# Kernel optimization log

Hardware: AMD Instinct MI355X
Metric: run time of the kernel (lower is better)

## Reference

```python
import jax, jax.numpy as jnp
import numpy as np

BATCH = 65536
IN_A = 256
IN_B = 256
OUT = 64


def setup_inputs() -> dict:
    key = jax.random.key(0)
    k1, k2, k3, k4 = jax.random.split(key, 4)
    xa = jax.random.normal(k1, (BATCH, IN_A), dtype=jnp.float32)
    xb = jax.random.normal(k2, (BATCH, IN_B), dtype=jnp.float32)
    wa = jax.random.normal(k3, (IN_A, OUT), dtype=jnp.float32) * 0.05
    wb = jax.random.normal(k4, (IN_B, OUT), dtype=jnp.float32) * 0.05
    return {"xa": xa, "xb": xb, "wa": wa, "wb": wb}


def reference(xa, xb, wa, wb):
    # Plaintext semantics of the SSHE cross secret-shared matmul:
    # [z|rank_b] = [xa|rank_a] @ <wa> + [xb|rank_b] @ <wb>
    return xa @ wa + xb @ wb
```

## Files before the change

kernel.cpp:

```cpp
#include <hip/hip_runtime.h>
#include <stdint.h>


#define BATCH     65536
#define KH        256
#define NOUT      64
#define WT_SHORTS (512 * 64)
#define WT_BYTES  (WT_SHORTS * 2)

typedef __bf16 bf16x8 __attribute__((ext_vector_type(8)));
typedef float  f32x4  __attribute__((ext_vector_type(4)));


__global__ void prep_wt_kernel(const float* __restrict__ wa,
                               const float* __restrict__ wb,
                               __bf16* __restrict__ wt) {
    int t = blockIdx.x * 256 + threadIdx.x;
    int c = t & 63;
    int k = t >> 6;
    float va = wa[k * 64 + c];
    float vb = wb[k * 64 + c];
    int k2 = k + 256;
    wt[(k  >> 3) * 512 + c * 8 + (k  & 7)] = (__bf16)va;
    wt[(k2 >> 3) * 512 + c * 8 + (k2 & 7)] = (__bf16)vb;
}

template <bool USE_WS>
__global__ __launch_bounds__(512, 4)
void agg_gemm_kernel(const float* __restrict__ xa,
                     const float* __restrict__ xb,
                     const float* __restrict__ wa,
                     const float* __restrict__ wb,
                     const __bf16* __restrict__ wt,
                     float* __restrict__ out) {
    __shared__ __bf16 wlds[WT_SHORTS];
    const int t    = threadIdx.x;
    const int lane = t & 63;
    const int wave = t >> 6;

    if (USE_WS) {
        const f32x4* gsrc = (const f32x4*)wt;
        f32x4*       ldst = (f32x4*)&wlds[0];
        #pragma unroll
        for (int it = 0; it < 8; ++it) {
            ldst[it * 512 + t] = gsrc[it * 512 + t];
        }
    } else {
        int c  = t & 63;
        int kw = t >> 6;
        #pragma unroll
        for (int i = 0; i < 32; ++i) {
            int k  = kw * 32 + i;
            int k2 = k + 256;
            wlds[(k  >> 3) * 512 + c * 8 + (k  & 7)] = (__bf16)wa[k * 64 + c];
            wlds[(k2 >> 3) * 512 + c * 8 + (k2 & 7)] = (__bf16)wb[k * 64 + c];
        }
    }
    __syncthreads();

    const int gw   = blockIdx.x * 8 + wave;
    const int row  = gw * 16 + (lane & 15);
    const int kgrp = lane >> 4;
    const int kk   = kgrp * 8;

    const float* pa = xa + (size_t)row * 256 + kk;
    const float* pb = xb + (size_t)row * 256 + kk;

    f32x4 acc0 = {0.f, 0.f, 0.f, 0.f};
    f32x4 acc1 = acc0, acc2 = acc0, acc3 = acc0;

    #pragma unroll
    for (int step = 0; step < 16; ++step) {
        const int k0 = step * 32;
        const float* px = (step < 8) ? (pa + k0) : (pb + (k0 - 256));
        f32x4 x0 = *(const f32x4*)(px);
        f32x4 x1 = *(const f32x4*)(px + 4);
        bf16x8 af;
        af[0] = (__bf16)x0[0]; af[1] = (__bf16)x0[1];
        af[2] = (__bf16)x0[2]; af[3] = (__bf16)x0[3];
        af[4] = (__bf16)x1[0]; af[5] = (__bf16)x1[1];
        af[6] = (__bf16)x1[2]; af[7] = (__bf16)x1[3];

        const __bf16* bbase = &wlds[(step * 4 + kgrp) * 512 + (lane & 15) * 8];
        bf16x8 b0 = *(const bf16x8*)(bbase);
        bf16x8 b1 = *(const bf16x8*)(bbase + 16 * 8);
        bf16x8 b2 = *(const bf16x8*)(bbase + 32 * 8);
        bf16x8 b3 = *(const bf16x8*)(bbase + 48 * 8);

        acc0 = __builtin_amdgcn_mfma_f32_16x16x32_bf16(af, b0, acc0, 0, 0, 0);
        acc1 = __builtin_amdgcn_mfma_f32_16x16x32_bf16(af, b1, acc1, 0, 0, 0);
        acc2 = __builtin_amdgcn_mfma_f32_16x16x32_bf16(af, b2, acc2, 0, 0, 0);
        acc3 = __builtin_amdgcn_mfma_f32_16x16x32_bf16(af, b3, acc3, 0, 0, 0);
    }

    const int oc = lane & 15;
    float* po = out + (size_t)(gw * 16 + (lane >> 4) * 4) * 64 + oc;
    #pragma unroll
    for (int r = 0; r < 4; ++r) {
        po[r * 64 +  0] = acc0[r];
        po[r * 64 + 16] = acc1[r];
        po[r * 64 + 32] = acc2[r];
        po[r * 64 + 48] = acc3[r];
    }
}

extern "C" void kernel_launch(void* const* d_in, const int* in_sizes, int n_in,
                              void* d_out, int out_size, void* d_ws, size_t ws_size,
                              hipStream_t stream) {
    const float* xa = (const float*)d_in[0];
    const float* xb = (const float*)d_in[1];
    const float* wa = (const float*)d_in[2];
    const float* wb = (const float*)d_in[3];
    float* out = (float*)d_out;

    if (ws_size >= (size_t)WT_BYTES) {
        __bf16* wt = (__bf16*)d_ws;
        prep_wt_kernel<<<64, 256, 0, stream>>>(wa, wb, wt);
        agg_gemm_kernel<true><<<512, 512, 0, stream>>>(xa, xb, wa, wb, wt, out);
    } else {
        agg_gemm_kernel<false><<<512, 512, 0, stream>>>(xa, xb, wa, wb, nullptr, out);
    }
}
```

Baseline: 163.2 us.

## Stream activation tiles into LDS via async global_load_lds with double buffering

Activation rows are no longer loaded straight into registers from global memory. Each wave now stages 16x64-float chunks into a per-wave XOR-swizzled LDS buffer using global_load_lds, double buffered, with explicit vmcnt waits so the next chunk's loads overlap the MFMAs on the current one. The aim is better coalescing and latency hiding for the bandwidth-bound activation stream. In exchange it adds 64KB of LDS per block and drops the 4-block occupancy hint, so fewer blocks may be resident per CU.

New measurement: 159.2 us. -2.5%, faster.

```diff
diff --git a/kernel.cpp b/kernel.cpp
--- a/kernel.cpp
+++ b/kernel.cpp
@@ -2,15 +2,11 @@
 #include <stdint.h>
 
 
-#define BATCH     65536
-#define KH        256
-#define NOUT      64
 #define WT_SHORTS (512 * 64)
 #define WT_BYTES  (WT_SHORTS * 2)
 
 typedef __bf16 bf16x8 __attribute__((ext_vector_type(8)));
 typedef float  f32x4  __attribute__((ext_vector_type(4)));
-
 
 __global__ void prep_wt_kernel(const float* __restrict__ wa,
                                const float* __restrict__ wb,
@@ -25,15 +21,23 @@
     wt[(k2 >> 3) * 512 + c * 8 + (k2 & 7)] = (__bf16)vb;
 }
 
+__device__ __forceinline__ void gload16(const void* g, void* l) {
+    __builtin_amdgcn_global_load_lds(
+        (const __attribute__((address_space(1))) void*)g,
+        (__attribute__((address_space(3))) void*)l, 16, 0, 0);
+}
+
 template <bool USE_WS>
-__global__ __launch_bounds__(512, 4)
+__global__ __launch_bounds__(512)
 void agg_gemm_kernel(const float* __restrict__ xa,
                      const float* __restrict__ xb,
                      const float* __restrict__ wa,
                      const float* __restrict__ wb,
                      const __bf16* __restrict__ wt,
                      float* __restrict__ out) {
-    __shared__ __bf16 wlds[WT_SHORTS];
+    __shared__ __align__(16) __bf16 wlds[WT_SHORTS];
+    __shared__ __align__(16) float xlds[2 * 8 * 1024];
+
     const int t    = threadIdx.x;
     const int lane = t & 63;
     const int wave = t >> 6;
@@ -42,9 +46,8 @@
         const f32x4* gsrc = (const f32x4*)wt;
         f32x4*       ldst = (f32x4*)&wlds[0];
         #pragma unroll
-        for (int it = 0; it < 8; ++it) {
+        for (int it = 0; it < 8; ++it)
             ldst[it * 512 + t] = gsrc[it * 512 + t];
-        }
     } else {
         int c  = t & 63;
         int kw = t >> 6;
@@ -59,42 +62,73 @@
     __syncthreads();
 
     const int gw   = blockIdx.x * 8 + wave;
-    const int row  = gw * 16 + (lane & 15);
+    const int tile = gw * 16;
+    const int row  = lane & 15;
     const int kgrp = lane >> 4;
-    const int kk   = kgrp * 8;
+    const int sw   = (row & 7) << 4;
 
-    const float* pa = xa + (size_t)row * 256 + kk;
-    const float* pb = xb + (size_t)row * 256 + kk;
+    char* xw0 = (char*)&xlds[(0 * 8 + wave) * 1024];
+    char* xw1 = (char*)&xlds[(1 * 8 + wave) * 1024];
+
+    const int r_lo = lane >> 4;
+    const int fk4  = (lane & 15) * 4;
+    auto stage = [&](int c) {
+        const float* srcm = (c < 4) ? xa : xb;
+        const int k0 = (c & 3) * 64;
+        char* ldsb = (c & 1) ? xw1 : xw0;
+        #pragma unroll
+        for (int j = 0; j < 4; ++j) {
+            int r = j * 4 + r_lo;
+            int f = fk4 ^ ((r & 7) << 2);
+            const float* g = srcm + (size_t)(tile + r) * 256 + k0 + f;
+            gload16(g, ldsb + j * 1024);
+        }
+    };
+
+    stage(0);
+    stage(1);
 
     f32x4 acc0 = {0.f, 0.f, 0.f, 0.f};
     f32x4 acc1 = acc0, acc2 = acc0, acc3 = acc0;
 
     #pragma unroll
-    for (int step = 0; step < 16; ++step) {
-        const int k0 = step * 32;
-        const float* px = (step < 8) ? (pa + k0) : (pb + (k0 - 256));
-        f32x4 x0 = *(const f32x4*)(px);
-        f32x4 x1 = *(const f32x4*)(px + 4);
-        bf16x8 af;
-        af[0] = (__bf16)x0[0]; af[1] = (__bf16)x0[1];
-        af[2] = (__bf16)x0[2]; af[3] = (__bf16)x0[3];
-        af[4] = (__bf16)x1[0]; af[5] = (__bf16)x1[1];
-        af[6] = (__bf16)x1[2]; af[7] = (__bf16)x1[3];
+    for (int c = 0; c < 8; ++c) {
+        if (c < 7) asm volatile("s_waitcnt vmcnt(4)" ::: "memory");
+        else       asm volatile("s_waitcnt vmcnt(0)" ::: "memory");
 
-        const __bf16* bbase = &wlds[(step * 4 + kgrp) * 512 + (lane & 15) * 8];
-        bf16x8 b0 = *(const bf16x8*)(bbase);
-        bf16x8 b1 = *(const bf16x8*)(bbase + 16 * 8);
-        bf16x8 b2 = *(const bf16x8*)(bbase + 32 * 8);
-        bf16x8 b3 = *(const bf16x8*)(bbase + 48 * 8);
+        const char* xbb = (c & 1) ? xw1 : xw0;
+        #pragma unroll
+        for (int sub = 0; sub < 2; ++sub) {
+            const int step = c * 2 + sub;
+            const int b0   = row * 256 + sub * 128 + kgrp * 32;
+            f32x4 x0 = *(const f32x4*)(xbb + (b0 ^ sw));
+            f32x4 x1 = *(const f32x4*)(xbb + ((b0 + 16) ^ sw));
+            bf16x8 af;
+            af[0] = (__bf16)x0[0]; af[1] = (__bf16)x0[1];
+            af[2] = (__bf16)x0[2]; af[3] = (__bf16)x0[3];
+            af[4] = (__bf16)x1[0]; af[5] = (__bf16)x1[1];
+            af[6] = (__bf16)x1[2]; af[7] = (__bf16)x1[3];
 
-        acc0 = __builtin_amdgcn_mfma_f32_16x16x32_bf16(af, b0, acc0, 0, 0, 0);
-        acc1 = __builtin_amdgcn_mfma_f32_16x16x32_bf16(af, b1, acc1, 0, 0, 0);
-        acc2 = __builtin_amdgcn_mfma_f32_16x16x32_bf16(af, b2, acc2, 0, 0, 0);
-        acc3 = __builtin_amdgcn_mfma_f32_16x16x32_bf16(af, b3, acc3, 0, 0, 0);
+            const __bf16* bbase = &wlds[(step * 4 + kgrp) * 512 + row * 8];
+            bf16x8 bf0 = *(const bf16x8*)(bbase);
+            bf16x8 bf1 = *(const bf16x8*)(bbase + 128);
+            bf16x8 bf2 = *(const bf16x8*)(bbase + 256);
+            bf16x8 bf3 = *(const bf16x8*)(bbase + 384);
+
+            acc0 = __builtin_amdgcn_mfma_f32_16x16x32_bf16(af, bf0, acc0, 0, 0, 0);
+            acc1 = __builtin_amdgcn_mfma_f32_16x16x32_bf16(af, bf1, acc1, 0, 0, 0);
+            acc2 = __builtin_amdgcn_mfma_f32_16x16x32_bf16(af, bf2, acc2, 0, 0, 0);
+            acc3 = __builtin_amdgcn_mfma_f32_16x16x32_bf16(af, bf3, acc3, 0, 0, 0);
+        }
+
+        if (c < 6) {
+            asm volatile("s_waitcnt lgkmcnt(0)" ::: "memory");
+            __builtin_amdgcn_sched_barrier(0);
+            stage(c + 2);
+        }
     }
 
-    const int oc = lane & 15;
-    float* po = out + (size_t)(gw * 16 + (lane >> 4) * 4) * 64 + oc;
+    float* po = out + (size_t)(tile + kgrp * 4) * 64 + row;
     #pragma unroll
     for (int r = 0; r < 4; ++r) {
         po[r * 64 +  0] = acc0[r];
```

## Prefetch activation rows four steps ahead and relayout weights for contiguous LDS reads

Applied to the files above, without the earlier changes.

The weight prep now writes the bf16 weights in exactly the per-lane fragment order the MFMA loop consumes, so each lane reads four contiguous 16-byte chunks at lane*8 offsets instead of a strided pattern. The main loop keeps a 4-deep register ring of activation loads, issuing global loads four k-steps ahead so memory latency overlaps the MFMAs. This costs extra VGPRs for the prefetch buffer, which may pressure occupancy under the 512x4 launch bounds.

Result: no change. 162.3 us (-0.6%).

```diff
diff --git a/kernel.cpp b/kernel.cpp
--- a/kernel.cpp
+++ b/kernel.cpp
@@ -2,27 +2,28 @@
 #include <stdint.h>
 
 
-#define BATCH     65536
-#define KH        256
-#define NOUT      64
 #define WT_SHORTS (512 * 64)
 #define WT_BYTES  (WT_SHORTS * 2)
 
 typedef __bf16 bf16x8 __attribute__((ext_vector_type(8)));
 typedef float  f32x4  __attribute__((ext_vector_type(4)));
 
-
 __global__ void prep_wt_kernel(const float* __restrict__ wa,
                                const float* __restrict__ wb,
                                __bf16* __restrict__ wt) {
-    int t = blockIdx.x * 256 + threadIdx.x;
-    int c = t & 63;
-    int k = t >> 6;
-    float va = wa[k * 64 + c];
-    float vb = wb[k * 64 + c];
-    int k2 = k + 256;
-    wt[(k  >> 3) * 512 + c * 8 + (k  & 7)] = (__bf16)va;
-    wt[(k2 >> 3) * 512 + c * 8 + (k2 & 7)] = (__bf16)vb;
+    int o2 = blockIdx.x * 256 + threadIdx.x;
+    #pragma unroll
+    for (int h = 0; h < 2; ++h) {
+        int o    = o2 * 2 + h;
+        int j    = o & 7;
+        int lane = (o >> 3) & 63;
+        int cb   = (o >> 9) & 3;
+        int s    = o >> 11;
+        int k    = s * 32 + (lane >> 4) * 8 + j;
+        int col  = (lane & 15) + cb * 16;
+        float v  = (k < 256) ? wa[k * 64 + col] : wb[(k - 256) * 64 + col];
+        wt[o] = (__bf16)v;
+    }
 }
 
 template <bool USE_WS>
@@ -33,68 +34,82 @@
                      const float* __restrict__ wb,
                      const __bf16* __restrict__ wt,
                      float* __restrict__ out) {
-    __shared__ __bf16 wlds[WT_SHORTS];
+    __shared__ __align__(16) __bf16 wlds[WT_SHORTS];
+
     const int t    = threadIdx.x;
     const int lane = t & 63;
     const int wave = t >> 6;
 
     if (USE_WS) {
-        const f32x4* gsrc = (const f32x4*)wt;
-        f32x4*       ldst = (f32x4*)&wlds[0];
+        const f32x4* g = (const f32x4*)wt;
+        f32x4*       l = (f32x4*)&wlds[0];
         #pragma unroll
-        for (int it = 0; it < 8; ++it) {
-            ldst[it * 512 + t] = gsrc[it * 512 + t];
-        }
+        for (int it = 0; it < 8; ++it)
+            l[it * 512 + t] = g[it * 512 + t];
     } else {
-        int c  = t & 63;
-        int kw = t >> 6;
-        #pragma unroll
-        for (int i = 0; i < 32; ++i) {
-            int k  = kw * 32 + i;
-            int k2 = k + 256;
-            wlds[(k  >> 3) * 512 + c * 8 + (k  & 7)] = (__bf16)wa[k * 64 + c];
-            wlds[(k2 >> 3) * 512 + c * 8 + (k2 & 7)] = (__bf16)wb[k * 64 + c];
+        for (int i = 0; i < 64; ++i) {
+            int o    = t * 64 + i;
+            int j    = o & 7;
+            int ln   = (o >> 3) & 63;
+            int cb   = (o >> 9) & 3;
+            int s    = o >> 11;
+            int k    = s * 32 + (ln >> 4) * 8 + j;
+            int col  = (ln & 15) + cb * 16;
+            wlds[o] = (__bf16)((k < 256) ? wa[k * 64 + col] : wb[(k - 256) * 64 + col]);
         }
     }
     __syncthreads();
 
     const int gw   = blockIdx.x * 8 + wave;
-    const int row  = gw * 16 + (lane & 15);
-    const int kgrp = lane >> 4;
-    const int kk   = kgrp * 8;
+    const int tile = gw * 16;
+    const int row  = lane & 15;
+    const int kg   = lane >> 4;
 
-    const float* pa = xa + (size_t)row * 256 + kk;
-    const float* pb = xb + (size_t)row * 256 + kk;
+    const float* prow_a = xa + (size_t)(tile + row) * 256 + kg * 8;
+    const float* prow_b = xb + (size_t)(tile + row) * 256 + kg * 8;
+
+    f32x4 xr[4][2];
+    #pragma unroll
+    for (int s = 0; s < 4; ++s) {
+        xr[s][0] = *(const f32x4*)(prow_a + s * 32);
+        xr[s][1] = *(const f32x4*)(prow_a + s * 32 + 4);
+    }
 
     f32x4 acc0 = {0.f, 0.f, 0.f, 0.f};
     f32x4 acc1 = acc0, acc2 = acc0, acc3 = acc0;
 
     #pragma unroll
-    for (int step = 0; step < 16; ++step) {
-        const int k0 = step * 32;
-        const float* px = (step < 8) ? (pa + k0) : (pb + (k0 - 256));
-        f32x4 x0 = *(const f32x4*)(px);
-        f32x4 x1 = *(const f32x4*)(px + 4);
+    for (int s = 0; s < 16; ++s) {
+        f32x4 x0 = xr[s & 3][0];
+        f32x4 x1 = xr[s & 3][1];
+
+        if (s < 12) {
+            const int sp = s + 4;
+            const float* p = (sp < 8) ? (prow_a + sp * 32)
+                                      : (prow_b + (sp - 8) * 32);
+            xr[s & 3][0] = *(const f32x4*)(p);
+            xr[s & 3][1] = *(const f32x4*)(p + 4);
+        }
+
         bf16x8 af;
         af[0] = (__bf16)x0[0]; af[1] = (__bf16)x0[1];
         af[2] = (__bf16)x0[2]; af[3] = (__bf16)x0[3];
         af[4] = (__bf16)x1[0]; af[5] = (__bf16)x1[1];
         af[6] = (__bf16)x1[2]; af[7] = (__bf16)x1[3];
 
-        const __bf16* bbase = &wlds[(step * 4 + kgrp) * 512 + (lane & 15) * 8];
-        bf16x8 b0 = *(const bf16x8*)(bbase);
-        bf16x8 b1 = *(const bf16x8*)(bbase + 16 * 8);
-        bf16x8 b2 = *(const bf16x8*)(bbase + 32 * 8);
-        bf16x8 b3 = *(const bf16x8*)(bbase + 48 * 8);
+        const __bf16* wb0 = &wlds[(s * 4 + 0) * 512 + lane * 8];
+        bf16x8 w0 = *(const bf16x8*)(wb0);
+        bf16x8 w1 = *(const bf16x8*)(wb0 + 512);
+        bf16x8 w2 = *(const bf16x8*)(wb0 + 1024);
+        bf16x8 w3 = *(const bf16x8*)(wb0 + 1536);
 
-        acc0 = __builtin_amdgcn_mfma_f32_16x16x32_bf16(af, b0, acc0, 0, 0, 0);
-        acc1 = __builtin_amdgcn_mfma_f32_16x16x32_bf16(af, b1, acc1, 0, 0, 0);
-        acc2 = __builtin_amdgcn_mfma_f32_16x16x32_bf16(af, b2, acc2, 0, 0, 0);
-        acc3 = __builtin_amdgcn_mfma_f32_16x16x32_bf16(af, b3, acc3, 0, 0, 0);
+        acc0 = __builtin_amdgcn_mfma_f32_16x16x32_bf16(af, w0, acc0, 0, 0, 0);
+        acc1 = __builtin_amdgcn_mfma_f32_16x16x32_bf16(af, w1, acc1, 0, 0, 0);
+        acc2 = __builtin_amdgcn_mfma_f32_16x16x32_bf16(af, w2, acc2, 0, 0, 0);
+        acc3 = __builtin_amdgcn_mfma_f32_16x16x32_bf16(af, w3, acc3, 0, 0, 0);
     }
 
-    const int oc = lane & 15;
-    float* po = out + (size_t)(gw * 16 + (lane >> 4) * 4) * 64 + oc;
+    float* po = out + (size_t)(tile + kg * 4) * 64 + row;
     #pragma unroll
     for (int r = 0; r < 4; ++r) {
         po[r * 64 +  0] = acc0[r];
```
